# Optimization experiments

Hardware: AMD Instinct MI355X
Metric: run time of the kernel (lower is better)

## Reference

```python
import jax, jax.numpy as jnp
import numpy as np

D_MODEL = 1024
N_HEADS = 16
MAX_SEQ_LEN = 2048

def setup_inputs() -> dict:
    key = jax.random.key(0)
    ks = jax.random.split(key, 4)
    B, L, D = 2, 2048, D_MODEL
    s = 0.02
    x = jax.random.normal(ks[0], (B, L, D), dtype=jnp.float32)
    qkv_w = jax.random.normal(ks[1], (D, 3 * D), dtype=jnp.float32) * s
    qkv_b = jnp.zeros((3 * D,), dtype=jnp.float32)
    proj_w = jax.random.normal(ks[2], (D, D), dtype=jnp.float32) * s
    proj_b = jnp.zeros((D,), dtype=jnp.float32)
    bias_table = jax.random.normal(ks[3], (2 * MAX_SEQ_LEN - 1, N_HEADS), dtype=jnp.float32) * s
    return {"x": x, "qkv_w": qkv_w, "qkv_b": qkv_b, "proj_w": proj_w, "proj_b": proj_b, "bias_table": bias_table}

def reference(x, qkv_w, qkv_b, proj_w, proj_b, bias_table):
    B, L, D = x.shape
    H = N_HEADS
    dk = D // H
    scale = dk ** -0.5
    # fused qkv projection: (B,L,3,H,dk)
    qkv = (x @ qkv_w + qkv_b).reshape(B, L, 3, H, dk)
    q = qkv[:, :, 0].transpose(0, 2, 1, 3)  # (B,H,L,dk)
    k = qkv[:, :, 1].transpose(0, 2, 1, 3)
    v = qkv[:, :, 2].transpose(0, 2, 1, 3)
    attn = jnp.einsum("bhqd,bhkd->bhqk", q, k) * scale  # (B,H,L,L)
    # relative position bias gather (Swin-style)
    coords = jnp.arange(L)
    rel_idx = coords[None, :] - coords[:, None] + (MAX_SEQ_LEN - 1)  # (L,L)
    rel_bias = bias_table[rel_idx]  # (L,L,H)
    attn = attn + rel_bias.transpose(2, 0, 1)[None]  # (B,H,L,L)
    attn = jax.nn.softmax(attn, axis=-1)
    out = jnp.einsum("bhqk,bhkd->bhqd", attn, v)  # (B,H,L,dk)
    out = out.transpose(0, 2, 1, 3).reshape(B, L, D)
    return out @ proj_w + proj_b
```

## Files before the change

### kernel.cpp

```cpp
#include <hip/hip_runtime.h>
#include <stdint.h>

typedef __attribute__((ext_vector_type(4))) float    f32x4;
typedef f32x4 __attribute__((aligned(4)))   f32x4u;
typedef __attribute__((ext_vector_type(8))) short    bf16x8;
typedef __attribute__((ext_vector_type(2))) uint32_t u32x2;

#define MFMA16(a,b,c) __builtin_amdgcn_mfma_f32_16x16x32_bf16((a),(b),(c),0,0,0)

__device__ __forceinline__ uint16_t f2bf(float f){
  uint32_t u = __float_as_uint(f);
  return (uint16_t)((u + 0x7FFFu + ((u >> 16) & 1u)) >> 16);
}

__device__ __forceinline__ uint32_t pk_bf16(float lo, float hi){
  uint32_t r; asm("v_cvt_pk_bf16_f32 %0, %1, %2" : "=v"(r) : "v"(lo), "v"(hi)); return r;
}

__device__ __forceinline__ float fast_exp2(float x){
  float r; asm("v_exp_f32 %0, %1" : "=v"(r) : "v"(x)); return r;
}

__device__ __forceinline__ void gload16(const uint16_t* g, uint16_t* l){
  __builtin_amdgcn_global_load_lds((const __attribute__((address_space(1))) uint32_t*)g,
                                   (__attribute__((address_space(3))) uint32_t*)l, 16, 0, 0);
}

__global__ void k_cvt(const float* __restrict__ in, uint16_t* __restrict__ out){
  const size_t i = (size_t)(blockIdx.x*256 + threadIdx.x) * 4;
  const f32x4 v = *(const f32x4*)(in + i);
  u32x2 pk = {pk_bf16(v[0], v[1]), pk_bf16(v[2], v[3])};
  *(u32x2*)(out + i) = pk;
}

__global__ void k_tcvt(const float* __restrict__ in, uint16_t* __restrict__ out, int K, int N){
  __shared__ float tile[64][65];
  const int k0 = blockIdx.y*64, n0 = blockIdx.x*64;
  const int tc = threadIdx.x & 63, tr = threadIdx.x >> 6;
  #pragma unroll
  for (int p=0;p<16;p++){ int r = p*4 + tr; tile[r][tc] = in[(size_t)(k0+r)*N + n0 + tc]; }
  __syncthreads();
  #pragma unroll
  for (int p=0;p<16;p++){ int r = p*4 + tr; out[(size_t)(n0+r)*K + k0 + tc] = f2bf(tile[tc][r]); }
}

__global__ void k_biast(const float* __restrict__ in, float* __restrict__ out){
  const int i = blockIdx.x*256 + threadIdx.x;
  if (i < 4095*16) out[(i & 15)*4096 + (i >> 4)] = in[i] * 1.4426950408889634f;
}

template<int EPI>
__global__ __launch_bounds__(256, 2) void k_gemm(
    const uint16_t* __restrict__ A, const uint16_t* __restrict__ Bt,
    const float* __restrict__ bias,
    uint16_t* __restrict__ qo, uint16_t* __restrict__ ko, uint16_t* __restrict__ vto,
    float* __restrict__ outf)
{
  __shared__ __align__(16) uint16_t at[128*64];
  __shared__ __align__(16) uint16_t bt[128*64];
  const int tid = threadIdx.x;
  const int lane = tid & 63, w = tid >> 6;
  const int g = lane >> 4, li = lane & 15;
  const int wr = w >> 1, wc = w & 1;
  const int m0 = blockIdx.y * 128, n0 = blockIdx.x * 128;

  f32x4 acc[4][4] = {};

  const int srow = tid >> 3;
  const int scg  = (tid & 7) ^ (srow & 7);

  for (int kt_ = 0; kt_ < 16; kt_++){
    const int kk = kt_*64;
    __syncthreads();
    #pragma unroll
    for (int j = 0; j < 4; j++){
      gload16(A  + (size_t)(m0 + j*32 + srow)*1024 + kk + scg*8, at + (j*256+tid)*8);
      gload16(Bt + (size_t)(n0 + j*32 + srow)*1024 + kk + scg*8, bt + (j*256+tid)*8);
    }
    asm volatile("s_waitcnt vmcnt(0)" ::: "memory");
    __syncthreads();

    bf16x8 af[2][4], bfr[2][4];
    #pragma unroll
    for (int mi=0; mi<4; mi++){
      int row = wr*64 + mi*16 + li, sw = row & 7;
      af[0][mi] = *(const bf16x8*)(at + row*64 + ((g     ^ sw)*8));
      af[1][mi] = *(const bf16x8*)(at + row*64 + (((4+g) ^ sw)*8));
    }
    #pragma unroll
    for (int ni=0; ni<4; ni++){
      int row = wc*64 + ni*16 + li, sw = row & 7;
      bfr[0][ni] = *(const bf16x8*)(bt + row*64 + ((g     ^ sw)*8));
      bfr[1][ni] = *(const bf16x8*)(bt + row*64 + (((4+g) ^ sw)*8));
    }
    #pragma unroll
    for (int s=0; s<2; s++)
      #pragma unroll
      for (int mi=0; mi<4; mi++)
        #pragma unroll
        for (int ni=0; ni<4; ni++)
          acc[mi][ni] = MFMA16(af[s][mi], bfr[s][ni], acc[mi][ni]);
  }

  if (EPI == 0){
    #pragma unroll
    for (int ni=0; ni<4; ni++){
      const int c = n0 + wc*64 + ni*16 + li;
      const float bv = bias[c];
      const int which = c >> 10, cc = c & 1023;
      const int h = cc >> 6, d = cc & 63;
      #pragma unroll
      for (int mi=0; mi<4; mi++){
        const int trow = m0 + wr*64 + mi*16 + g*4;
        const int b_ = trow >> 11, lcl = trow & 2047;
        const f32x4 v4 = acc[mi][ni];
        if (which == 0){
          uint16_t* dst = qo + (((size_t)(b_*16 + h)*2048 + lcl)*64 + d);
          #pragma unroll
          for (int r=0;r<4;r++) dst[(size_t)r*64] = f2bf((v4[r] + bv) * 0.18033688011112042f);
        } else if (which == 1){
          uint16_t* dst = ko + (((size_t)(b_*16 + h)*2048 + lcl)*64 + d);
          #pragma unroll
          for (int r=0;r<4;r++) dst[(size_t)r*64] = f2bf(v4[r] + bv);
        } else {
          u32x2 pk = {pk_bf16(v4[0]+bv, v4[1]+bv), pk_bf16(v4[2]+bv, v4[3]+bv)};
          *(u32x2*)(vto + (((size_t)(b_*16 + h)*64 + d)*2048 + lcl)) = pk;
        }
      }
    }
  } else {
    #pragma unroll
    for (int ni=0; ni<4; ni++){
      const int c = n0 + wc*64 + ni*16 + li;
      const float bv = bias[c];
      #pragma unroll
      for (int mi=0; mi<4; mi++){
        const int trow = m0 + wr*64 + mi*16 + g*4;
        float* dst = outf + (size_t)trow*1024 + c;
        const f32x4 v4 = acc[mi][ni];
        #pragma unroll
        for (int r=0;r<4;r++) dst[(size_t)r*1024] = v4[r] + bv;
      }
    }
  }
}

__device__ __forceinline__ void attn_tile(
    int t, bool last, int tid, int g, int li, int srow, int scg,
    const uint16_t* kbase, const uint16_t* vbase, const float* bb,
    const uint16_t* ktc, uint16_t* ktn, const uint16_t* vtc, uint16_t* vtn, uint16_t* pl,
    const bf16x8 (&qf)[2][2], bf16x8 ones,
    f32x4 (&o)[4][2], f32x4 (&o4)[2], float& mrun0, float& mrun1,
    const f32x4 (&bvC)[2][4], f32x4 (&bvN)[2][4])
{
  if (!last){
    const int kv1 = (t+1)*64;
    gload16(kbase + (size_t)(kv1+srow)*64 + scg*8,         ktn + tid*8);
    gload16(kbase + (size_t)(kv1+srow+32)*64 + scg*8,      ktn + 2048 + tid*8);
    gload16(vbase + (size_t)srow*2048 + kv1 + scg*8,       vtn + tid*8);
    gload16(vbase + (size_t)(srow+32)*2048 + kv1 + scg*8,  vtn + 2048 + tid*8);
    #pragma unroll
    for (int c=0;c<2;c++)
      #pragma unroll
      for (int mf=0;mf<4;mf++)
        bvN[c][mf] = *(const f32x4u*)(bb + kv1 + mf*16 + g*4 - c*16 - li);
    asm volatile("s_waitcnt vmcnt(12)" ::: "memory");
  } else {
    asm volatile("s_waitcnt vmcnt(0)" ::: "memory");
  }
  __builtin_amdgcn_s_barrier();

  f32x4 sa[4][2];
  __builtin_amdgcn_s_setprio(1);
  #pragma unroll
  for (int mf=0; mf<4; mf++){
    const int row = mf*16 + li, sw = row & 7;
    bf16x8 a0 = *(const bf16x8*)(ktc + row*64 + ((g     ^ sw)*8));
    bf16x8 a1 = *(const bf16x8*)(ktc + row*64 + (((4+g) ^ sw)*8));
    #pragma unroll
    for (int c=0;c<2;c++){
      f32x4 cfr = {};
      cfr = MFMA16(a0, qf[c][0], cfr);
      cfr = MFMA16(a1, qf[c][1], cfr);
      sa[mf][c] = cfr;
    }
  }
  __builtin_amdgcn_s_setprio(0);

  float t0 = -__builtin_inff(), t1 = -__builtin_inff();
  #pragma unroll
  for (int mf=0; mf<4; mf++){
    sa[mf][0] += bvC[0][mf];
    sa[mf][1] += bvC[1][mf];
    #pragma unroll
    for (int r=0; r<4; r++){
      t0 = fmaxf(t0, sa[mf][0][r]);
      t1 = fmaxf(t1, sa[mf][1][r]);
    }
  }

  const int ok = (t0 <= mrun0 + 8.f) && (t1 <= mrun1 + 8.f);
  if (!__all(ok)){
    float r0 = t0, r1 = t1;
    r0 = fmaxf(r0, __shfl_xor(r0, 16)); r0 = fmaxf(r0, __shfl_xor(r0, 32));
    r1 = fmaxf(r1, __shfl_xor(r1, 16)); r1 = fmaxf(r1, __shfl_xor(r1, 32));
    const float mn0 = fmaxf(mrun0, r0), mn1 = fmaxf(mrun1, r1);
    const float a0 = fast_exp2(mrun0 - mn0), a1 = fast_exp2(mrun1 - mn1);
    #pragma unroll
    for (int mf=0; mf<4; mf++){ o[mf][0] *= a0; o[mf][1] *= a1; }
    o4[0] *= a0; o4[1] *= a1;
    mrun0 = mn0; mrun1 = mn1;
  }

  const int swp2 = 2*(li & 7);
  #pragma unroll
  for (int c=0;c<2;c++){
    const float mr = c ? mrun1 : mrun0;
    #pragma unroll
    for (int mf=0; mf<4; mf++){
      float p0 = fast_exp2(sa[mf][c][0] - mr);
      float p1 = fast_exp2(sa[mf][c][1] - mr);
      float p2 = fast_exp2(sa[mf][c][2] - mr);
      float p3 = fast_exp2(sa[mf][c][3] - mr);
      u32x2 pk = {pk_bf16(p0,p1), pk_bf16(p2,p3)};
      *(u32x2*)(pl + (c*16+li)*64 + (((4*mf+g) ^ swp2)*4)) = pk;
    }
  }

  bf16x8 av[2][4];
  #pragma unroll
  for (int s=0; s<2; s++)
    #pragma unroll
    for (int mf=0; mf<4; mf++){
      const int row = mf*16 + li, sw = row & 7;
      av[s][mf] = *(const bf16x8*)(vtc + row*64 + (((4*s+g) ^ sw)*8));
    }
  __builtin_amdgcn_s_setprio(1);
  #pragma unroll
  for (int c=0;c<2;c++){
    #pragma unroll
    for (int s=0; s<2; s++){
      bf16x8 pb = *(const bf16x8*)(pl + (c*16+li)*64 + (((8*s+2*g) ^ swp2)*4));
      o4[c] = MFMA16(ones, pb, o4[c]);
      #pragma unroll
      for (int mf=0; mf<4; mf++)
        o[mf][c] = MFMA16(av[s][mf], pb, o[mf][c]);
    }
  }
  __builtin_amdgcn_s_setprio(0);
  __builtin_amdgcn_s_barrier();
}

__global__ __launch_bounds__(256, 2) void k_attn(
    const uint16_t* __restrict__ qg, const uint16_t* __restrict__ kg,
    const uint16_t* __restrict__ vg, const float* __restrict__ biast,
    uint16_t* __restrict__ outp)
{
  __shared__ __align__(16) uint16_t kt[2][64*64];
  __shared__ __align__(16) uint16_t vt[2][64*64];
  __shared__ __align__(16) uint16_t pt[4][32*64];
  const int tid = threadIdx.x;
  const int lane = tid & 63, w = tid >> 6;
  const int g = lane >> 4, li = lane & 15;
  const int bh = blockIdx.y, h = bh & 15, b_ = bh >> 4;
  const int qb0 = blockIdx.x * 128;
  const int qw = qb0 + w*32;

  bf16x8 qf[2][2];
  #pragma unroll
  for (int c=0;c<2;c++){
    const uint16_t* qp = qg + ((size_t)bh*2048 + qw + c*16 + li)*64 + g*8;
    qf[c][0] = *(const bf16x8*)(qp);
    qf[c][1] = *(const bf16x8*)(qp + 32);
  }
  bf16x8 ones = (bf16x8)(short)0;
  if (li == 0){ const short v = (short)0x3F80; ones = (bf16x8){v,v,v,v,v,v,v,v}; }

  f32x4 o[4][2] = {};
  f32x4 o4[2] = {};
  float mrun0 = -__builtin_inff(), mrun1 = -__builtin_inff();

  const uint16_t* kbase = kg + (size_t)bh*(2048*64);
  const uint16_t* vbase = vg + (size_t)bh*(64*2048);
  const int srow = tid >> 3;
  const int scg  = (tid & 7) ^ (srow & 7);
  const float* bb = biast + h*4096 + 2047 - qw;
  uint16_t* pl = &pt[w][0];

  gload16(kbase + (size_t)srow*64 + scg*8,         &kt[0][tid*8]);
  gload16(kbase + (size_t)(srow+32)*64 + scg*8,    &kt[0][2048 + tid*8]);
  gload16(vbase + (size_t)srow*2048 + scg*8,       &vt[0][tid*8]);
  gload16(vbase + (size_t)(srow+32)*2048 + scg*8,  &vt[0][2048 + tid*8]);
  f32x4 bvA[2][4], bvB[2][4];
  #pragma unroll
  for (int c=0;c<2;c++)
    #pragma unroll
    for (int mf=0;mf<4;mf++)
      bvA[c][mf] = *(const f32x4u*)(bb + mf*16 + g*4 - c*16 - li);

  for (int tt = 0; tt < 32; tt += 2){
    attn_tile(tt,   false,    tid, g, li, srow, scg, kbase, vbase, bb,
              &kt[0][0], &kt[1][0], &vt[0][0], &vt[1][0], pl,
              qf, ones, o, o4, mrun0, mrun1, bvA, bvB);
    attn_tile(tt+1, tt == 30, tid, g, li, srow, scg, kbase, vbase, bb,
              &kt[1][0], &kt[0][0], &vt[1][0], &vt[0][0], pl,
              qf, ones, o, o4, mrun0, mrun1, bvB, bvA);
  }

  const float ls0 = __shfl(o4[0][0], li);
  const float ls1 = __shfl(o4[1][0], li);
  const float inv0 = 1.0f / ls0, inv1 = 1.0f / ls1;
  #pragma unroll
  for (int c=0;c<2;c++){
    const float inv = c ? inv1 : inv0;
    const size_t token = (size_t)b_*2048 + qw + c*16 + li;
    #pragma unroll
    for (int mf=0; mf<4; mf++){
      u32x2 pk = {pk_bf16(o[mf][c][0]*inv, o[mf][c][1]*inv),
                  pk_bf16(o[mf][c][2]*inv, o[mf][c][3]*inv)};
      *(u32x2*)(outp + token*1024 + h*64 + mf*16 + g*4) = pk;
    }
  }
}

extern "C" void kernel_launch(void* const* d_in, const int* in_sizes, int n_in,
                              void* d_out, int out_size, void* d_ws, size_t ws_size,
                              hipStream_t stream)
{
  const float* x      = (const float*)d_in[0];
  const float* qkv_w  = (const float*)d_in[1];
  const float* qkv_b  = (const float*)d_in[2];
  const float* proj_w = (const float*)d_in[3];
  const float* proj_b = (const float*)d_in[4];
  const float* btab   = (const float*)d_in[5];
  float* out = (float*)d_out;

  char* p = (char*)d_ws;
  uint16_t* x_bf    = (uint16_t*)(p);
  uint16_t* qkv_wt  = (uint16_t*)(p + 8388608);
  uint16_t* proj_wt = (uint16_t*)(p + 14680064);
  uint16_t* q_buf   = (uint16_t*)(p + 16777216);
  uint16_t* k_buf   = (uint16_t*)(p + 25165824);
  uint16_t* vt_buf  = (uint16_t*)(p + 33554432);
  uint16_t* ao_buf  = (uint16_t*)(p + 41943040);
  float*    bias_t  = (float*)   (p + 50331648);

  k_cvt  <<<dim3(4096),  dim3(256), 0, stream>>>(x, x_bf);
  k_tcvt <<<dim3(48,16), dim3(256), 0, stream>>>(qkv_w,  qkv_wt,  1024, 3072);
  k_tcvt <<<dim3(16,16), dim3(256), 0, stream>>>(proj_w, proj_wt, 1024, 1024);
  k_biast<<<dim3(256),   dim3(256), 0, stream>>>(btab, bias_t);

  k_gemm<0><<<dim3(24,32), dim3(256), 0, stream>>>(x_bf, qkv_wt, qkv_b, q_buf, k_buf, vt_buf, nullptr);
  k_attn   <<<dim3(16,32), dim3(256), 0, stream>>>(q_buf, k_buf, vt_buf, bias_t, ao_buf);
  k_gemm<1><<<dim3(8,32),  dim3(256), 0, stream>>>(ao_buf, proj_wt, proj_b, nullptr, nullptr, nullptr, out);
}
```

Baseline: 128.4 us.

## Halve attention block to two waves and double grid with interleaved query blocks

The attention kernel now runs 128-thread blocks, each covering 64 query rows, and the grid doubles to 32x32. Each thread issues four K and four V async loads per tile instead of two, and the vmcnt threshold rises to match. Query blocks are remapped through an interleaved blockIdx permutation. The aim is more blocks to fill the CUs and less imbalance in the tail, at the cost of twice the K/V tile loads per query row and lower K/V reuse per block.

```diff
diff --git a/kernel.cpp b/kernel.cpp
--- a/kernel.cpp
+++ b/kernel.cpp
@@ -146,7 +146,7 @@
 }
 
 __device__ __forceinline__ void attn_tile(
-    int t, bool last, int tid, int g, int li, int srow, int scg,
+    int t, bool last, int tid, int g, int li, int srow16, int scg,
     const uint16_t* kbase, const uint16_t* vbase, const float* bb,
     const uint16_t* ktc, uint16_t* ktn, const uint16_t* vtc, uint16_t* vtn, uint16_t* pl,
     const bf16x8 (&qf)[2][2], bf16x8 ones,
@@ -155,16 +155,17 @@
 {
   if (!last){
     const int kv1 = (t+1)*64;
-    gload16(kbase + (size_t)(kv1+srow)*64 + scg*8,         ktn + tid*8);
-    gload16(kbase + (size_t)(kv1+srow+32)*64 + scg*8,      ktn + 2048 + tid*8);
-    gload16(vbase + (size_t)srow*2048 + kv1 + scg*8,       vtn + tid*8);
-    gload16(vbase + (size_t)(srow+32)*2048 + kv1 + scg*8,  vtn + 2048 + tid*8);
+    #pragma unroll
+    for (int j=0;j<4;j++){
+      gload16(kbase + (size_t)(kv1+srow16+16*j)*64 + scg*8,      ktn + j*1024 + tid*8);
+      gload16(vbase + (size_t)(srow16+16*j)*2048 + kv1 + scg*8,  vtn + j*1024 + tid*8);
+    }
     #pragma unroll
     for (int c=0;c<2;c++)
       #pragma unroll
       for (int mf=0;mf<4;mf++)
         bvN[c][mf] = *(const f32x4u*)(bb + kv1 + mf*16 + g*4 - c*16 - li);
-    asm volatile("s_waitcnt vmcnt(12)" ::: "memory");
+    asm volatile("s_waitcnt vmcnt(16)" ::: "memory");
   } else {
     asm volatile("s_waitcnt vmcnt(0)" ::: "memory");
   }
@@ -251,20 +252,21 @@
   __builtin_amdgcn_s_barrier();
 }
 
-__global__ __launch_bounds__(256, 2) void k_attn(
+__global__ __launch_bounds__(128, 2) void k_attn(
     const uint16_t* __restrict__ qg, const uint16_t* __restrict__ kg,
     const uint16_t* __restrict__ vg, const float* __restrict__ biast,
     uint16_t* __restrict__ outp)
 {
   __shared__ __align__(16) uint16_t kt[2][64*64];
   __shared__ __align__(16) uint16_t vt[2][64*64];
-  __shared__ __align__(16) uint16_t pt[4][32*64];
+  __shared__ __align__(16) uint16_t pt[2][32*64];
   const int tid = threadIdx.x;
   const int lane = tid & 63, w = tid >> 6;
   const int g = lane >> 4, li = lane & 15;
   const int bh = blockIdx.y, h = bh & 15, b_ = bh >> 4;
-  const int qb0 = blockIdx.x * 128;
-  const int qw = qb0 + w*32;
+  const int bx = blockIdx.x;
+  const int qx = (bx >> 3) + 4*(bx & 7);
+  const int qw = qx*64 + w*32;
 
   bf16x8 qf[2][2];
   #pragma unroll
@@ -282,15 +284,16 @@
 
   const uint16_t* kbase = kg + (size_t)bh*(2048*64);
   const uint16_t* vbase = vg + (size_t)bh*(64*2048);
-  const int srow = tid >> 3;
-  const int scg  = (tid & 7) ^ (srow & 7);
+  const int srow16 = tid >> 3;
+  const int scg    = (tid & 7) ^ (srow16 & 7);
   const float* bb = biast + h*4096 + 2047 - qw;
   uint16_t* pl = &pt[w][0];
 
-  gload16(kbase + (size_t)srow*64 + scg*8,         &kt[0][tid*8]);
-  gload16(kbase + (size_t)(srow+32)*64 + scg*8,    &kt[0][2048 + tid*8]);
-  gload16(vbase + (size_t)srow*2048 + scg*8,       &vt[0][tid*8]);
-  gload16(vbase + (size_t)(srow+32)*2048 + scg*8,  &vt[0][2048 + tid*8]);
+  #pragma unroll
+  for (int j=0;j<4;j++){
+    gload16(kbase + (size_t)(srow16+16*j)*64 + scg*8,        &kt[0][j*1024 + tid*8]);
+    gload16(vbase + (size_t)(srow16+16*j)*2048 + scg*8,      &vt[0][j*1024 + tid*8]);
+  }
   f32x4 bvA[2][4], bvB[2][4];
   #pragma unroll
   for (int c=0;c<2;c++)
@@ -299,10 +302,10 @@
       bvA[c][mf] = *(const f32x4u*)(bb + mf*16 + g*4 - c*16 - li);
 
   for (int tt = 0; tt < 32; tt += 2){
-    attn_tile(tt,   false,    tid, g, li, srow, scg, kbase, vbase, bb,
+    attn_tile(tt,   false,    tid, g, li, srow16, scg, kbase, vbase, bb,
               &kt[0][0], &kt[1][0], &vt[0][0], &vt[1][0], pl,
               qf, ones, o, o4, mrun0, mrun1, bvA, bvB);
-    attn_tile(tt+1, tt == 30, tid, g, li, srow, scg, kbase, vbase, bb,
+    attn_tile(tt+1, tt == 30, tid, g, li, srow16, scg, kbase, vbase, bb,
               &kt[1][0], &kt[0][0], &vt[1][0], &vt[0][0], pl,
               qf, ones, o, o4, mrun0, mrun1, bvB, bvA);
   }
@@ -351,6 +354,6 @@
   k_biast<<<dim3(256),   dim3(256), 0, stream>>>(btab, bias_t);
 
   k_gemm<0><<<dim3(24,32), dim3(256), 0, stream>>>(x_bf, qkv_wt, qkv_b, q_buf, k_buf, vt_buf, nullptr);
-  k_attn   <<<dim3(16,32), dim3(256), 0, stream>>>(q_buf, k_buf, vt_buf, bias_t, ao_buf);
+  k_attn   <<<dim3(32,32), dim3(128), 0, stream>>>(q_buf, k_buf, vt_buf, bias_t, ao_buf);
   k_gemm<1><<<dim3(8,32),  dim3(256), 0, stream>>>(ao_buf, proj_wt, proj_b, nullptr, nullptr, nullptr, out);
 }
```

Result: no change. 130.2 us (+1.5%).

## Load K/V fragments directly from global into registers in attention, drop LDS staging

Applied to the files above, without the earlier changes.

Removes the shared-memory double buffers for K and V tiles and their barriers. Each wave now loads its MFMA operand fragments for K and V straight from global memory into registers, prefetching the next K tile while softmax runs. Bias is loaded as five overlapping vectors instead of eight per tile. The grid is flattened so consecutive blocks cover different heads for the same query chunk. This trades block-level synchronisation and LDS traffic for four times redundant global/L2 reads of K/V across the waves of a block, plus longer exposed latency on V loads.

```diff
diff --git a/kernel.cpp b/kernel.cpp
--- a/kernel.cpp
+++ b/kernel.cpp
@@ -145,126 +145,19 @@
   }
 }
 
-__device__ __forceinline__ void attn_tile(
-    int t, bool last, int tid, int g, int li, int srow, int scg,
-    const uint16_t* kbase, const uint16_t* vbase, const float* bb,
-    const uint16_t* ktc, uint16_t* ktn, const uint16_t* vtc, uint16_t* vtn, uint16_t* pl,
-    const bf16x8 (&qf)[2][2], bf16x8 ones,
-    f32x4 (&o)[4][2], f32x4 (&o4)[2], float& mrun0, float& mrun1,
-    const f32x4 (&bvC)[2][4], f32x4 (&bvN)[2][4])
-{
-  if (!last){
-    const int kv1 = (t+1)*64;
-    gload16(kbase + (size_t)(kv1+srow)*64 + scg*8,         ktn + tid*8);
-    gload16(kbase + (size_t)(kv1+srow+32)*64 + scg*8,      ktn + 2048 + tid*8);
-    gload16(vbase + (size_t)srow*2048 + kv1 + scg*8,       vtn + tid*8);
-    gload16(vbase + (size_t)(srow+32)*2048 + kv1 + scg*8,  vtn + 2048 + tid*8);
-    #pragma unroll
-    for (int c=0;c<2;c++)
-      #pragma unroll
-      for (int mf=0;mf<4;mf++)
-        bvN[c][mf] = *(const f32x4u*)(bb + kv1 + mf*16 + g*4 - c*16 - li);
-    asm volatile("s_waitcnt vmcnt(12)" ::: "memory");
-  } else {
-    asm volatile("s_waitcnt vmcnt(0)" ::: "memory");
-  }
-  __builtin_amdgcn_s_barrier();
-
-  f32x4 sa[4][2];
-  __builtin_amdgcn_s_setprio(1);
-  #pragma unroll
-  for (int mf=0; mf<4; mf++){
-    const int row = mf*16 + li, sw = row & 7;
-    bf16x8 a0 = *(const bf16x8*)(ktc + row*64 + ((g     ^ sw)*8));
-    bf16x8 a1 = *(const bf16x8*)(ktc + row*64 + (((4+g) ^ sw)*8));
-    #pragma unroll
-    for (int c=0;c<2;c++){
-      f32x4 cfr = {};
-      cfr = MFMA16(a0, qf[c][0], cfr);
-      cfr = MFMA16(a1, qf[c][1], cfr);
-      sa[mf][c] = cfr;
-    }
-  }
-  __builtin_amdgcn_s_setprio(0);
-
-  float t0 = -__builtin_inff(), t1 = -__builtin_inff();
-  #pragma unroll
-  for (int mf=0; mf<4; mf++){
-    sa[mf][0] += bvC[0][mf];
-    sa[mf][1] += bvC[1][mf];
-    #pragma unroll
-    for (int r=0; r<4; r++){
-      t0 = fmaxf(t0, sa[mf][0][r]);
-      t1 = fmaxf(t1, sa[mf][1][r]);
-    }
-  }
-
-  const int ok = (t0 <= mrun0 + 8.f) && (t1 <= mrun1 + 8.f);
-  if (!__all(ok)){
-    float r0 = t0, r1 = t1;
-    r0 = fmaxf(r0, __shfl_xor(r0, 16)); r0 = fmaxf(r0, __shfl_xor(r0, 32));
-    r1 = fmaxf(r1, __shfl_xor(r1, 16)); r1 = fmaxf(r1, __shfl_xor(r1, 32));
-    const float mn0 = fmaxf(mrun0, r0), mn1 = fmaxf(mrun1, r1);
-    const float a0 = fast_exp2(mrun0 - mn0), a1 = fast_exp2(mrun1 - mn1);
-    #pragma unroll
-    for (int mf=0; mf<4; mf++){ o[mf][0] *= a0; o[mf][1] *= a1; }
-    o4[0] *= a0; o4[1] *= a1;
-    mrun0 = mn0; mrun1 = mn1;
-  }
-
-  const int swp2 = 2*(li & 7);
-  #pragma unroll
-  for (int c=0;c<2;c++){
-    const float mr = c ? mrun1 : mrun0;
-    #pragma unroll
-    for (int mf=0; mf<4; mf++){
-      float p0 = fast_exp2(sa[mf][c][0] - mr);
-      float p1 = fast_exp2(sa[mf][c][1] - mr);
-      float p2 = fast_exp2(sa[mf][c][2] - mr);
-      float p3 = fast_exp2(sa[mf][c][3] - mr);
-      u32x2 pk = {pk_bf16(p0,p1), pk_bf16(p2,p3)};
-      *(u32x2*)(pl + (c*16+li)*64 + (((4*mf+g) ^ swp2)*4)) = pk;
-    }
-  }
-
-  bf16x8 av[2][4];
-  #pragma unroll
-  for (int s=0; s<2; s++)
-    #pragma unroll
-    for (int mf=0; mf<4; mf++){
-      const int row = mf*16 + li, sw = row & 7;
-      av[s][mf] = *(const bf16x8*)(vtc + row*64 + (((4*s+g) ^ sw)*8));
-    }
-  __builtin_amdgcn_s_setprio(1);
-  #pragma unroll
-  for (int c=0;c<2;c++){
-    #pragma unroll
-    for (int s=0; s<2; s++){
-      bf16x8 pb = *(const bf16x8*)(pl + (c*16+li)*64 + (((8*s+2*g) ^ swp2)*4));
-      o4[c] = MFMA16(ones, pb, o4[c]);
-      #pragma unroll
-      for (int mf=0; mf<4; mf++)
-        o[mf][c] = MFMA16(av[s][mf], pb, o[mf][c]);
-    }
-  }
-  __builtin_amdgcn_s_setprio(0);
-  __builtin_amdgcn_s_barrier();
-}
-
 __global__ __launch_bounds__(256, 2) void k_attn(
     const uint16_t* __restrict__ qg, const uint16_t* __restrict__ kg,
     const uint16_t* __restrict__ vg, const float* __restrict__ biast,
     uint16_t* __restrict__ outp)
 {
-  __shared__ __align__(16) uint16_t kt[2][64*64];
-  __shared__ __align__(16) uint16_t vt[2][64*64];
   __shared__ __align__(16) uint16_t pt[4][32*64];
   const int tid = threadIdx.x;
   const int lane = tid & 63, w = tid >> 6;
   const int g = lane >> 4, li = lane & 15;
-  const int bh = blockIdx.y, h = bh & 15, b_ = bh >> 4;
-  const int qb0 = blockIdx.x * 128;
-  const int qw = qb0 + w*32;
+  const int id = blockIdx.x;
+  const int bh = id & 31, qxi = id >> 5;
+  const int h = bh & 15, b_ = bh >> 4;
+  const int qw = qxi*128 + w*32;
 
   bf16x8 qf[2][2];
   #pragma unroll
@@ -282,29 +175,107 @@
 
   const uint16_t* kbase = kg + (size_t)bh*(2048*64);
   const uint16_t* vbase = vg + (size_t)bh*(64*2048);
-  const int srow = tid >> 3;
-  const int scg  = (tid & 7) ^ (srow & 7);
   const float* bb = biast + h*4096 + 2047 - qw;
   uint16_t* pl = &pt[w][0];
-
-  gload16(kbase + (size_t)srow*64 + scg*8,         &kt[0][tid*8]);
-  gload16(kbase + (size_t)(srow+32)*64 + scg*8,    &kt[0][2048 + tid*8]);
-  gload16(vbase + (size_t)srow*2048 + scg*8,       &vt[0][tid*8]);
-  gload16(vbase + (size_t)(srow+32)*2048 + scg*8,  &vt[0][2048 + tid*8]);
-  f32x4 bvA[2][4], bvB[2][4];
-  #pragma unroll
-  for (int c=0;c<2;c++)
-    #pragma unroll
-    for (int mf=0;mf<4;mf++)
-      bvA[c][mf] = *(const f32x4u*)(bb + mf*16 + g*4 - c*16 - li);
-
-  for (int tt = 0; tt < 32; tt += 2){
-    attn_tile(tt,   false,    tid, g, li, srow, scg, kbase, vbase, bb,
-              &kt[0][0], &kt[1][0], &vt[0][0], &vt[1][0], pl,
-              qf, ones, o, o4, mrun0, mrun1, bvA, bvB);
-    attn_tile(tt+1, tt == 30, tid, g, li, srow, scg, kbase, vbase, bb,
-              &kt[1][0], &kt[0][0], &vt[1][0], &vt[0][0], pl,
-              qf, ones, o, o4, mrun0, mrun1, bvB, bvA);
+  const int swp2 = 2*(li & 7);
+
+  bf16x8 k0[4], k1[4];
+  #pragma unroll
+  for (int mf=0; mf<4; mf++){
+    const uint16_t* kp = kbase + (size_t)(mf*16 + li)*64 + g*8;
+    k0[mf] = *(const bf16x8*)(kp);
+    k1[mf] = *(const bf16x8*)(kp + 32);
+  }
+
+  for (int t = 0; t < 32; t++){
+    const int kv0 = t*64;
+    const int kv1 = ((t+1) & 31)*64;
+
+    bf16x8 v0[4], v1[4];
+    #pragma unroll
+    for (int mf=0; mf<4; mf++){
+      const uint16_t* vp = vbase + (size_t)(mf*16 + li)*2048 + kv0 + g*8;
+      v0[mf] = *(const bf16x8*)(vp);
+      v1[mf] = *(const bf16x8*)(vp + 32);
+    }
+    f32x4 bv5[5];
+    #pragma unroll
+    for (int j=0; j<5; j++)
+      bv5[j] = *(const f32x4u*)(bb + kv0 + (j-1)*16 + g*4 - li);
+
+    f32x4 sa[4][2];
+    __builtin_amdgcn_s_setprio(1);
+    #pragma unroll
+    for (int mf=0; mf<4; mf++){
+      #pragma unroll
+      for (int c=0;c<2;c++){
+        f32x4 cfr = {};
+        cfr = MFMA16(k0[mf], qf[c][0], cfr);
+        cfr = MFMA16(k1[mf], qf[c][1], cfr);
+        sa[mf][c] = cfr;
+      }
+    }
+    __builtin_amdgcn_s_setprio(0);
+
+    #pragma unroll
+    for (int mf=0; mf<4; mf++){
+      const uint16_t* kp = kbase + (size_t)(kv1 + mf*16 + li)*64 + g*8;
+      k0[mf] = *(const bf16x8*)(kp);
+      k1[mf] = *(const bf16x8*)(kp + 32);
+    }
+
+    float t0 = -__builtin_inff(), t1 = -__builtin_inff();
+    #pragma unroll
+    for (int mf=0; mf<4; mf++){
+      sa[mf][0] += bv5[mf+1];
+      sa[mf][1] += bv5[mf];
+      #pragma unroll
+      for (int r=0; r<4; r++){
+        t0 = fmaxf(t0, sa[mf][0][r]);
+        t1 = fmaxf(t1, sa[mf][1][r]);
+      }
+    }
+
+    const int ok = (t0 <= mrun0 + 8.f) && (t1 <= mrun1 + 8.f);
+    if (!__all(ok)){
+      float r0 = t0, r1 = t1;
+      r0 = fmaxf(r0, __shfl_xor(r0, 16)); r0 = fmaxf(r0, __shfl_xor(r0, 32));
+      r1 = fmaxf(r1, __shfl_xor(r1, 16)); r1 = fmaxf(r1, __shfl_xor(r1, 32));
+      const float mn0 = fmaxf(mrun0, r0), mn1 = fmaxf(mrun1, r1);
+      const float a0 = fast_exp2(mrun0 - mn0), a1 = fast_exp2(mrun1 - mn1);
+      #pragma unroll
+      for (int mf=0; mf<4; mf++){ o[mf][0] *= a0; o[mf][1] *= a1; }
+      o4[0] *= a0; o4[1] *= a1;
+      mrun0 = mn0; mrun1 = mn1;
+    }
+
+    #pragma unroll
+    for (int c=0;c<2;c++){
+      const float mr = c ? mrun1 : mrun0;
+      #pragma unroll
+      for (int mf=0; mf<4; mf++){
+        float p0 = fast_exp2(sa[mf][c][0] - mr);
+        float p1 = fast_exp2(sa[mf][c][1] - mr);
+        float p2 = fast_exp2(sa[mf][c][2] - mr);
+        float p3 = fast_exp2(sa[mf][c][3] - mr);
+        u32x2 pk = {pk_bf16(p0,p1), pk_bf16(p2,p3)};
+        *(u32x2*)(pl + (c*16+li)*64 + (((4*mf+g) ^ swp2)*4)) = pk;
+      }
+    }
+
+    __builtin_amdgcn_s_setprio(1);
+    #pragma unroll
+    for (int c=0;c<2;c++){
+      #pragma unroll
+      for (int s=0; s<2; s++){
+        bf16x8 pb = *(const bf16x8*)(pl + (c*16+li)*64 + (((8*s+2*g) ^ swp2)*4));
+        o4[c] = MFMA16(ones, pb, o4[c]);
+        #pragma unroll
+        for (int mf=0; mf<4; mf++)
+          o[mf][c] = MFMA16(s ? v1[mf] : v0[mf], pb, o[mf][c]);
+      }
+    }
+    __builtin_amdgcn_s_setprio(0);
   }
 
   const float ls0 = __shfl(o4[0][0], li);
@@ -351,6 +322,6 @@
   k_biast<<<dim3(256),   dim3(256), 0, stream>>>(btab, bias_t);
 
   k_gemm<0><<<dim3(24,32), dim3(256), 0, stream>>>(x_bf, qkv_wt, qkv_b, q_buf, k_buf, vt_buf, nullptr);
-  k_attn   <<<dim3(16,32), dim3(256), 0, stream>>>(q_buf, k_buf, vt_buf, bias_t, ao_buf);
+  k_attn   <<<dim3(512),   dim3(256), 0, stream>>>(q_buf, k_buf, vt_buf, bias_t, ao_buf);
   k_gemm<1><<<dim3(8,32),  dim3(256), 0, stream>>>(ao_buf, proj_wt, proj_b, nullptr, nullptr, nullptr, out);
 }
```

New measurement: 193.8 us. 1.51x slower.

## Split attention KV range in two and merge partials with log-sum-exp

Applied to the files above, without the earlier changes.

The attention kernel now splits the 2048-key range into two halves per query block, doubling the grid, and writes normalized partial outputs plus per-row log-sum-exp values. A new merge kernel combines the two partials with softmax weights into the attention output buffer. The P staging buffer is halved by processing one query column group at a time, and launch bounds are raised to 4 waves per SIMD to raise occupancy. Partials go in scratch space (d_out and the start of the workspace), which adds extra memory traffic, a launch, and bf16 rounding of the partials.

```diff
diff --git a/kernel.cpp b/kernel.cpp
--- a/kernel.cpp
+++ b/kernel.cpp
@@ -5,6 +5,7 @@
 typedef f32x4 __attribute__((aligned(4)))   f32x4u;
 typedef __attribute__((ext_vector_type(8))) short    bf16x8;
 typedef __attribute__((ext_vector_type(2))) uint32_t u32x2;
+typedef __attribute__((ext_vector_type(4))) uint32_t u32x4;
 
 #define MFMA16(a,b,c) __builtin_amdgcn_mfma_f32_16x16x32_bf16((a),(b),(c),0,0,0)
 
@@ -20,6 +21,12 @@
 __device__ __forceinline__ float fast_exp2(float x){
   float r; asm("v_exp_f32 %0, %1" : "=v"(r) : "v"(x)); return r;
 }
+__device__ __forceinline__ float fast_log2(float x){
+  float r; asm("v_log_f32 %0, %1" : "=v"(r) : "v"(x)); return r;
+}
+
+__device__ __forceinline__ float bfl(uint32_t u){ return __uint_as_float(u << 16); }
+__device__ __forceinline__ float bfh(uint32_t u){ return __uint_as_float(u & 0xffff0000u); }
 
 __device__ __forceinline__ void gload16(const uint16_t* g, uint16_t* l){
   __builtin_amdgcn_global_load_lds((const __attribute__((address_space(1))) uint32_t*)g,
@@ -164,7 +171,7 @@
       #pragma unroll
       for (int mf=0;mf<4;mf++)
         bvN[c][mf] = *(const f32x4u*)(bb + kv1 + mf*16 + g*4 - c*16 - li);
-    asm volatile("s_waitcnt vmcnt(12)" ::: "memory");
+    asm volatile("s_waitcnt vmcnt(16)" ::: "memory");
   } else {
     asm volatile("s_waitcnt vmcnt(0)" ::: "memory");
   }
@@ -212,6 +219,15 @@
     mrun0 = mn0; mrun1 = mn1;
   }
 
+  bf16x8 av[2][4];
+  #pragma unroll
+  for (int s=0; s<2; s++)
+    #pragma unroll
+    for (int mf=0; mf<4; mf++){
+      const int row = mf*16 + li, sw = row & 7;
+      av[s][mf] = *(const bf16x8*)(vtc + row*64 + (((4*s+g) ^ sw)*8));
+    }
+
   const int swp2 = 2*(li & 7);
   #pragma unroll
   for (int c=0;c<2;c++){
@@ -223,48 +239,38 @@
       float p2 = fast_exp2(sa[mf][c][2] - mr);
       float p3 = fast_exp2(sa[mf][c][3] - mr);
       u32x2 pk = {pk_bf16(p0,p1), pk_bf16(p2,p3)};
-      *(u32x2*)(pl + (c*16+li)*64 + (((4*mf+g) ^ swp2)*4)) = pk;
-    }
-  }
-
-  bf16x8 av[2][4];
-  #pragma unroll
-  for (int s=0; s<2; s++)
-    #pragma unroll
-    for (int mf=0; mf<4; mf++){
-      const int row = mf*16 + li, sw = row & 7;
-      av[s][mf] = *(const bf16x8*)(vtc + row*64 + (((4*s+g) ^ sw)*8));
-    }
-  __builtin_amdgcn_s_setprio(1);
-  #pragma unroll
-  for (int c=0;c<2;c++){
+      *(u32x2*)(pl + li*64 + (((4*mf+g) ^ swp2)*4)) = pk;
+    }
+    __builtin_amdgcn_s_setprio(1);
     #pragma unroll
     for (int s=0; s<2; s++){
-      bf16x8 pb = *(const bf16x8*)(pl + (c*16+li)*64 + (((8*s+2*g) ^ swp2)*4));
+      bf16x8 pb = *(const bf16x8*)(pl + li*64 + (((8*s+2*g) ^ swp2)*4));
       o4[c] = MFMA16(ones, pb, o4[c]);
       #pragma unroll
       for (int mf=0; mf<4; mf++)
         o[mf][c] = MFMA16(av[s][mf], pb, o[mf][c]);
     }
-  }
-  __builtin_amdgcn_s_setprio(0);
+    __builtin_amdgcn_s_setprio(0);
+  }
   __builtin_amdgcn_s_barrier();
 }
 
-__global__ __launch_bounds__(256, 2) void k_attn(
+__global__ __launch_bounds__(256, 4) void k_attn(
     const uint16_t* __restrict__ qg, const uint16_t* __restrict__ kg,
     const uint16_t* __restrict__ vg, const float* __restrict__ biast,
-    uint16_t* __restrict__ outp)
+    uint16_t* __restrict__ opart, float* __restrict__ spart)
 {
   __shared__ __align__(16) uint16_t kt[2][64*64];
   __shared__ __align__(16) uint16_t vt[2][64*64];
-  __shared__ __align__(16) uint16_t pt[4][32*64];
+  __shared__ __align__(16) uint16_t pt[4][16*64];
   const int tid = threadIdx.x;
   const int lane = tid & 63, w = tid >> 6;
   const int g = lane >> 4, li = lane & 15;
   const int bh = blockIdx.y, h = bh & 15, b_ = bh >> 4;
-  const int qb0 = blockIdx.x * 128;
-  const int qw = qb0 + w*32;
+  const int id = blockIdx.x;
+  const int split = id & 1, qxi = id >> 1;
+  const int qw = qxi*128 + w*32;
+  const int tg0 = split*16;
 
   bf16x8 qf[2][2];
   #pragma unroll
@@ -287,22 +293,23 @@
   const float* bb = biast + h*4096 + 2047 - qw;
   uint16_t* pl = &pt[w][0];
 
-  gload16(kbase + (size_t)srow*64 + scg*8,         &kt[0][tid*8]);
-  gload16(kbase + (size_t)(srow+32)*64 + scg*8,    &kt[0][2048 + tid*8]);
-  gload16(vbase + (size_t)srow*2048 + scg*8,       &vt[0][tid*8]);
-  gload16(vbase + (size_t)(srow+32)*2048 + scg*8,  &vt[0][2048 + tid*8]);
+  const int kvp = tg0*64;
+  gload16(kbase + (size_t)(kvp+srow)*64 + scg*8,        &kt[0][tid*8]);
+  gload16(kbase + (size_t)(kvp+srow+32)*64 + scg*8,     &kt[0][2048 + tid*8]);
+  gload16(vbase + (size_t)srow*2048 + kvp + scg*8,      &vt[0][tid*8]);
+  gload16(vbase + (size_t)(srow+32)*2048 + kvp + scg*8, &vt[0][2048 + tid*8]);
   f32x4 bvA[2][4], bvB[2][4];
   #pragma unroll
   for (int c=0;c<2;c++)
     #pragma unroll
     for (int mf=0;mf<4;mf++)
-      bvA[c][mf] = *(const f32x4u*)(bb + mf*16 + g*4 - c*16 - li);
-
-  for (int tt = 0; tt < 32; tt += 2){
-    attn_tile(tt,   false,    tid, g, li, srow, scg, kbase, vbase, bb,
+      bvA[c][mf] = *(const f32x4u*)(bb + kvp + mf*16 + g*4 - c*16 - li);
+
+  for (int tt = 0; tt < 16; tt += 2){
+    attn_tile(tg0+tt,   false,      tid, g, li, srow, scg, kbase, vbase, bb,
               &kt[0][0], &kt[1][0], &vt[0][0], &vt[1][0], pl,
               qf, ones, o, o4, mrun0, mrun1, bvA, bvB);
-    attn_tile(tt+1, tt == 30, tid, g, li, srow, scg, kbase, vbase, bb,
+    attn_tile(tg0+tt+1, tt == 14,   tid, g, li, srow, scg, kbase, vbase, bb,
               &kt[1][0], &kt[0][0], &vt[1][0], &vt[0][0], pl,
               qf, ones, o, o4, mrun0, mrun1, bvB, bvA);
   }
@@ -310,17 +317,43 @@
   const float ls0 = __shfl(o4[0][0], li);
   const float ls1 = __shfl(o4[1][0], li);
   const float inv0 = 1.0f / ls0, inv1 = 1.0f / ls1;
+  const float sv0 = mrun0 + fast_log2(ls0);
+  const float sv1 = mrun1 + fast_log2(ls1);
   #pragma unroll
   for (int c=0;c<2;c++){
     const float inv = c ? inv1 : inv0;
-    const size_t token = (size_t)b_*2048 + qw + c*16 + li;
+    const int token = b_*2048 + qw + c*16 + li;
+    if (g == 0) spart[split*65536 + token*16 + h] = c ? sv1 : sv0;
+    uint16_t* dst = opart + ((size_t)(split*4096 + token))*1024 + h*64;
     #pragma unroll
     for (int mf=0; mf<4; mf++){
       u32x2 pk = {pk_bf16(o[mf][c][0]*inv, o[mf][c][1]*inv),
                   pk_bf16(o[mf][c][2]*inv, o[mf][c][3]*inv)};
-      *(u32x2*)(outp + token*1024 + h*64 + mf*16 + g*4) = pk;
-    }
-  }
+      *(u32x2*)(dst + mf*16 + g*4) = pk;
+    }
+  }
+}
+
+__global__ void k_merge(const uint16_t* __restrict__ op, const float* __restrict__ sp,
+                        uint16_t* __restrict__ ao){
+  const int gid = blockIdx.x*256 + threadIdx.x;
+  const int token = gid >> 7, col0 = (gid & 127) * 8, h = col0 >> 6;
+  const float s0 = sp[token*16 + h], s1 = sp[65536 + token*16 + h];
+  const float sm = fmaxf(s0, s1);
+  float w0 = fast_exp2(s0 - sm), w1 = fast_exp2(s1 - sm);
+  const float inv = 1.0f / (w0 + w1);
+  w0 *= inv; w1 *= inv;
+  const size_t i0 = (size_t)token*1024 + col0;
+  const u32x4 a = *(const u32x4*)(op + i0);
+  const u32x4 b = *(const u32x4*)(op + (size_t)4096*1024 + i0);
+  u32x4 r;
+  #pragma unroll
+  for (int j=0;j<4;j++){
+    const float e0 = w0*bfl(a[j]) + w1*bfl(b[j]);
+    const float e1 = w0*bfh(a[j]) + w1*bfh(b[j]);
+    r[j] = pk_bf16(e0, e1);
+  }
+  *(u32x4*)(ao + i0) = r;
 }
 
 extern "C" void kernel_launch(void* const* d_in, const int* in_sizes, int n_in,
@@ -345,12 +378,16 @@
   uint16_t* ao_buf  = (uint16_t*)(p + 41943040);
   float*    bias_t  = (float*)   (p + 50331648);
 
+  uint16_t* o_part = (uint16_t*)d_out;
+  float*    s_part = (float*)p;
+
   k_cvt  <<<dim3(4096),  dim3(256), 0, stream>>>(x, x_bf);
   k_tcvt <<<dim3(48,16), dim3(256), 0, stream>>>(qkv_w,  qkv_wt,  1024, 3072);
   k_tcvt <<<dim3(16,16), dim3(256), 0, stream>>>(proj_w, proj_wt, 1024, 1024);
   k_biast<<<dim3(256),   dim3(256), 0, stream>>>(btab, bias_t);
 
   k_gemm<0><<<dim3(24,32), dim3(256), 0, stream>>>(x_bf, qkv_wt, qkv_b, q_buf, k_buf, vt_buf, nullptr);
-  k_attn   <<<dim3(16,32), dim3(256), 0, stream>>>(q_buf, k_buf, vt_buf, bias_t, ao_buf);
+  k_attn   <<<dim3(32,32), dim3(256), 0, stream>>>(q_buf, k_buf, vt_buf, bias_t, o_part, s_part);
+  k_merge  <<<dim3(2048),  dim3(256), 0, stream>>>(o_part, s_part, ao_buf);
   k_gemm<1><<<dim3(8,32),  dim3(256), 0, stream>>>(ao_buf, proj_wt, proj_b, nullptr, nullptr, nullptr, out);
 }
```

New measurement: 403.7 us. +214.5%, slower.
